# Kernel tuning notes

Hardware: AMD Instinct MI355X
Metric: run time of the kernel (lower is better)

The kernel has to match this reference:

```python
import jax, jax.numpy as jnp
import numpy as np

D_MODEL = 256
D_STATE = 64
D_CONV = 4
EXPAND = 2
HEADDIM = 64
D_INNER = EXPAND * D_MODEL            # 512
NHEADS = D_INNER // HEADDIM           # 8
D_XBC = D_INNER + 2 * D_STATE         # 640 (x, B, C; ngroups=1)
D_IN_PROJ = 2 * D_INNER + 2 * D_STATE + NHEADS  # 1160


def setup_inputs() -> dict:
    key = jax.random.key(0)
    ks = jax.random.split(key, 8)
    x = jax.random.normal(ks[0], (64, 5000, 12), jnp.float32)
    W_in = jax.random.normal(ks[1], (D_MODEL, D_IN_PROJ), jnp.float32) * 0.02
    conv_w = jax.random.normal(ks[2], (D_XBC, D_CONV), jnp.float32) * 0.1
    conv_b = jnp.zeros((D_XBC,), jnp.float32)
    A_log = jnp.log(jax.random.uniform(ks[3], (NHEADS,), jnp.float32, 1.0, 16.0))
    dt_bias = jax.random.normal(ks[4], (NHEADS,), jnp.float32) * 0.1
    D = jnp.ones((NHEADS,), jnp.float32)
    norm_w = jnp.ones((D_INNER,), jnp.float32)
    W_out = jax.random.normal(ks[5], (D_INNER, D_MODEL), jnp.float32) * 0.02
    return {"x": x, "W_in": W_in, "conv_w": conv_w, "conv_b": conv_b,
            "A_log": A_log, "dt_bias": dt_bias, "D": D,
            "norm_w": norm_w, "W_out": W_out}


def _mamba2(u, W_in, conv_w, conv_b, A_log, dt_bias, D, norm_w, W_out):
    b, l, _ = u.shape
    zxbcdt = u @ W_in                                   # (b,l,1160)
    z = zxbcdt[..., :D_INNER]                           # (b,l,512)
    xBC = zxbcdt[..., D_INNER:D_INNER + D_XBC]          # (b,l,640)
    dt = zxbcdt[..., D_INNER + D_XBC:]                  # (b,l,8)
    # causal depthwise conv1d (kernel 4) + SiLU
    xp = jnp.pad(xBC, ((0, 0), (D_CONV - 1, 0), (0, 0)))
    xBC = sum(xp[:, k:k + l, :] * conv_w[:, k] for k in range(D_CONV)) + conv_b
    xBC = jax.nn.silu(xBC)
    xs = xBC[..., :D_INNER].reshape(b, l, NHEADS, HEADDIM)
    Bm = xBC[..., D_INNER:D_INNER + D_STATE]            # (b,l,64)
    Cm = xBC[..., D_INNER + D_STATE:]                   # (b,l,64)
    dt = jax.nn.softplus(dt + dt_bias)                  # (b,l,h)
    A = -jnp.exp(A_log)                                 # (h,)

    def step(h, inp):
        x_t, dt_t, B_t, C_t = inp                       # (b,h,p),(b,h),(b,n),(b,n)
        decay = jnp.exp(dt_t * A)                       # (b,h)
        h = h * decay[..., None, None] + (dt_t[..., None] * x_t)[..., None] * B_t[:, None, None, :]
        y = jnp.einsum('bhpn,bn->bhp', h, C_t)
        return h, y

    h0 = jnp.zeros((b, NHEADS, HEADDIM, D_STATE), u.dtype)
    _, ys = jax.lax.scan(step, h0, (xs.transpose(1, 0, 2, 3), dt.transpose(1, 0, 2),
                                    Bm.transpose(1, 0, 2), Cm.transpose(1, 0, 2)))
    y = ys.transpose(1, 0, 2, 3) + D[None, None, :, None] * xs   # D skip, per head
    y = y.reshape(b, l, D_INNER)
    # RMSNormGated: gate then rmsnorm
    y = y * jax.nn.silu(z)
    y = y * jax.lax.rsqrt(jnp.mean(y * y, axis=-1, keepdims=True) + 1e-5) * norm_w
    return y @ W_out                                    # (b,l,256)


def reference(x, W_in, conv_w, conv_b, A_log, dt_bias, D, norm_w, W_out):
    b = x.shape[0]
    u = x.reshape(b, 250, 240)                          # 'b (t p1) f -> b t (p1 f)'
    u = jnp.pad(u, ((0, 0), (0, 0), (0, D_MODEL - 240)))
    y = _mamba2(u, W_in, conv_w, conv_b, A_log, dt_bias, D, norm_w, W_out)
    y = jax.nn.selu(y)                                  # AlphaDropout is identity at eval
    y = y[..., :240]
    return y.reshape(b, 5000, 12)
```

## Files before the change

### kernel.cpp

```cpp
#include <hip/hip_runtime.h>
#include <cstdint>
#include <cstddef>

#define D_MODEL 256
#define D_STATE 64
#define HEADDIM 64
#define D_INNER 512
#define NHEADS 8
#define D_XBC 640
#define NPROJ 1160
#define ZXW 1152
#define BATCH 64
#define SEQ 250
#define ROWS (BATCH * SEQ)
#define KIN 240
#define KPAD 256
#define NPAD 1216
#define TPAD 256

typedef __bf16 bf16x8 __attribute__((ext_vector_type(8)));
typedef float f32x4 __attribute__((ext_vector_type(4)));

__device__ __forceinline__ float readlane_f(float v, int lane) {
    return __uint_as_float(__builtin_amdgcn_readlane(__float_as_uint(v), lane));
}
__device__ __forceinline__ float silu_f(float x) { return x * (1.f / (1.f + __expf(-x))); }
__device__ __forceinline__ unsigned short bf16_rne(float f) {
    unsigned int u = __float_as_uint(f);
    u += 0x7fff + ((u >> 16) & 1);
    return (unsigned short)(u >> 16);
}
__device__ __forceinline__ float bf2f(unsigned short u) {
    return __uint_as_float(((unsigned int)u) << 16);
}
__device__ __forceinline__ unsigned int pack2(float a, float b) {
    return (unsigned int)bf16_rne(a) | ((unsigned int)bf16_rne(b) << 16);
}

__global__ __launch_bounds__(256) void cast_w_kernel(const float* __restrict__ Win,
                                                     unsigned short* __restrict__ bt_bf) {
    int idx = blockIdx.x * 256 + threadIdx.x;
    int n = idx >> 8, k = idx & 255;
    float v = (n < NPROJ && k < KIN) ? Win[k * NPROJ + n] : 0.f;
    bt_bf[idx] = bf16_rne(v);
}

#define SA 40
__global__ __launch_bounds__(256) void gemm1_mfma(const float* __restrict__ X,
                                                  const unsigned short* __restrict__ Bt,
                                                  unsigned short* __restrict__ Czx,
                                                  float* __restrict__ dtraw) {
    __shared__ unsigned short As[128 * SA];
    __shared__ unsigned short Bs[64 * SA];
    const int tid = threadIdx.x;
    const int lane = tid & 63, wave = tid >> 6;
    const int wm = wave >> 1, wn = wave & 1;
    const int q = lane >> 4, l15 = lane & 15;
    const int rowBase = blockIdx.y * 128, colBase = blockIdx.x * 64;
    f32x4 acc[4][2] = {};

    const int sr = tid >> 2;
    const int sc = (tid & 3) * 8;

    for (int k0 = 0; k0 < KPAD; k0 += 32) {
        const int kseg = k0 + sc;
        const bool kv = kseg < KIN;
        {
            unsigned short tmp[8] = {0, 0, 0, 0, 0, 0, 0, 0};
            if (kv) {
                const float* xr = X + (size_t)(rowBase + sr) * KIN + kseg;
                float4 a = *(const float4*)&xr[0];
                float4 b2 = *(const float4*)&xr[4];
                tmp[0] = bf16_rne(a.x); tmp[1] = bf16_rne(a.y);
                tmp[2] = bf16_rne(a.z); tmp[3] = bf16_rne(a.w);
                tmp[4] = bf16_rne(b2.x); tmp[5] = bf16_rne(b2.y);
                tmp[6] = bf16_rne(b2.z); tmp[7] = bf16_rne(b2.w);
            }
            *(uint4*)&As[sr * SA + sc] = *(uint4*)tmp;
        }
        {
            unsigned short tmp[8] = {0, 0, 0, 0, 0, 0, 0, 0};
            if (kv) {
                const float* xr = X + (size_t)(rowBase + sr + 64) * KIN + kseg;
                float4 a = *(const float4*)&xr[0];
                float4 b2 = *(const float4*)&xr[4];
                tmp[0] = bf16_rne(a.x); tmp[1] = bf16_rne(a.y);
                tmp[2] = bf16_rne(a.z); tmp[3] = bf16_rne(a.w);
                tmp[4] = bf16_rne(b2.x); tmp[5] = bf16_rne(b2.y);
                tmp[6] = bf16_rne(b2.z); tmp[7] = bf16_rne(b2.w);
            }
            *(uint4*)&As[(sr + 64) * SA + sc] = *(uint4*)tmp;
        }
        *(float4*)&Bs[sr * SA + sc] =
            *(const float4*)&Bt[(size_t)(colBase + sr) * KPAD + k0 + sc];
        __syncthreads();

        bf16x8 bfr[2];
#pragma unroll
        for (int nt = 0; nt < 2; nt++)
            bfr[nt] = *(const bf16x8*)&Bs[(wn * 32 + nt * 16 + l15) * SA + q * 8];
#pragma unroll
        for (int mt = 0; mt < 4; mt++) {
            bf16x8 afr = *(const bf16x8*)&As[(wm * 64 + mt * 16 + l15) * SA + q * 8];
#pragma unroll
            for (int nt = 0; nt < 2; nt++)
                acc[mt][nt] = __builtin_amdgcn_mfma_f32_16x16x32_bf16(afr, bfr[nt],
                                                                      acc[mt][nt], 0, 0, 0);
        }
        __syncthreads();
    }
#pragma unroll
    for (int mt = 0; mt < 4; mt++) {
        int grow0 = rowBase + wm * 64 + mt * 16 + q * 4;
#pragma unroll
        for (int nt = 0; nt < 2; nt++) {
            int gcol = colBase + wn * 32 + nt * 16 + l15;
            if (gcol < ZXW) {
#pragma unroll
                for (int reg = 0; reg < 4; reg++) {
                    unsigned int u = bf16_rne(acc[mt][nt][reg]);
                    unsigned int partner = (unsigned int)__shfl_xor((int)u, 1, 64);
                    if ((l15 & 1) == 0)
                        *(unsigned int*)&Czx[(size_t)(grow0 + reg) * ZXW + gcol] =
                            u | (partner << 16);
                }
            } else if (gcol < NPROJ) {
#pragma unroll
                for (int reg = 0; reg < 4; reg++)
                    dtraw[(size_t)(grow0 + reg) * NHEADS + (gcol - ZXW)] = acc[mt][nt][reg];
            }
        }
    }
}

#define CT_IN_STR 68
#define CT_TR_STR 70
__global__ __launch_bounds__(256) void conv_kernel(const unsigned short* __restrict__ zxbc,
                                                   const float* __restrict__ dtraw,
                                                   const float* __restrict__ conv_w,
                                                   const float* __restrict__ conv_b,
                                                   const float* __restrict__ dt_bias,
                                                   unsigned short* __restrict__ xc_bf,
                                                   unsigned short* __restrict__ xcT_bf,
                                                   float* __restrict__ dtp) {
    const int b = blockIdx.x;
    const int t0 = blockIdx.z * 64;
    if (blockIdx.y == 10) {
        for (int it = threadIdx.x; it < 512; it += 256) {
            int h = it & 7;
            int t = t0 + (it >> 3);
            if (t < SEQ) {
                float v = dtraw[(size_t)(b * SEQ + t) * NHEADS + h] + dt_bias[h];
                dtp[(size_t)(b * SEQ + t) * NHEADS + h] =
                    (v > 20.f) ? v : __logf(1.f + __expf(v));
            }
        }
        return;
    }
    __shared__ float In[67 * CT_IN_STR];
    __shared__ unsigned short OutT[64 * CT_TR_STR];
    const int cg = blockIdx.y;
    const int tid = threadIdx.x;
    const int lane = tid & 63;
    const int w = tid >> 6;
    const int ch = cg * 64 + lane;

    for (int r = w; r < 67; r += 4) {
        int t = t0 - 3 + r;
        float v = (t >= 0 && t < SEQ)
                      ? bf2f(zxbc[(size_t)(b * SEQ + t) * ZXW + D_INNER + ch])
                      : 0.f;
        In[r * CT_IN_STR + lane] = v;
    }
    __syncthreads();
    const float w0 = conv_w[ch * 4 + 0], w1 = conv_w[ch * 4 + 1];
    const float w2 = conv_w[ch * 4 + 2], w3 = conv_w[ch * 4 + 3];
    const float bias = conv_b[ch];
    unsigned short vals[16];
#pragma unroll
    for (int i = 0; i < 16; i++) {
        int tt = w * 16 + i;
        float acc = fmaf(w3, In[(tt + 3) * CT_IN_STR + lane],
                    fmaf(w2, In[(tt + 2) * CT_IN_STR + lane],
                    fmaf(w1, In[(tt + 1) * CT_IN_STR + lane],
                    fmaf(w0, In[tt * CT_IN_STR + lane], bias))));
        float sv = silu_f(acc);
        unsigned short bv = (t0 + tt < SEQ) ? bf16_rne(sv) : (unsigned short)0;
        vals[i] = bv;
        OutT[lane * CT_TR_STR + tt] = bv;
    }
#pragma unroll
    for (int i = 0; i < 16; i++) {
        int tt = w * 16 + i;
        if (t0 + tt < SEQ)
            xc_bf[(size_t)(b * SEQ + t0 + tt) * D_XBC + ch] = vals[i];
    }
    __syncthreads();
    unsigned short* dstbase = xcT_bf + ((size_t)b * D_XBC + cg * 64) * TPAD + t0;
#pragma unroll
    for (int i = 0; i < 16; i++) {
        int c2 = w * 16 + i;
        dstbase[(size_t)c2 * TPAD + lane] = OutT[c2 * CT_TR_STR + lane];
    }
}

#define LSTR 72
__global__ __launch_bounds__(256) void scan_intra(const unsigned short* __restrict__ xc_bf,
                                                  const unsigned short* __restrict__ xcT_bf,
                                                  const float* __restrict__ dtp,
                                                  const float* __restrict__ A_log,
                                                  const float* __restrict__ Dvec,
                                                  unsigned short* __restrict__ yout_bf,
                                                  unsigned short* __restrict__ st_g) {
    __shared__ unsigned short C_l[64 * LSTR];
    __shared__ unsigned short BP_l[64 * LSTR];
    __shared__ unsigned short XT_l[64 * LSTR];
    __shared__ float cs_s[64], dts_s[64], fws_s[64];

    const int blk = blockIdx.x;
    const int bh = blk >> 2, c = blk & 3;
    const int b = bh >> 3, h = bh & 7;
    const int tid = threadIdx.x;
    const int lane = tid & 63, w = tid >> 6;
    const int q = lane >> 4, l15 = lane & 15;
    const int t0 = c * 64;
    const float A = -__expf(A_log[h]);
    const float Dh = Dvec[h];

    const int r = tid >> 2, c0 = (tid & 3) * 16;

    {
        if (t0 + r < SEQ) {
            const unsigned short* rowp = xc_bf + (size_t)(b * SEQ + t0 + r) * D_XBC;
            *(uint4*)&C_l[r * LSTR + c0] = *(const uint4*)&rowp[D_INNER + D_STATE + c0];
            *(uint4*)&C_l[r * LSTR + c0 + 8] =
                *(const uint4*)&rowp[D_INNER + D_STATE + c0 + 8];
            *(uint4*)&BP_l[r * LSTR + c0] = *(const uint4*)&rowp[D_INNER + c0];
            *(uint4*)&BP_l[r * LSTR + c0 + 8] = *(const uint4*)&rowp[D_INNER + c0 + 8];
        } else {
            uint4 z = {0, 0, 0, 0};
            *(uint4*)&C_l[r * LSTR + c0] = z;
            *(uint4*)&C_l[r * LSTR + c0 + 8] = z;
            *(uint4*)&BP_l[r * LSTR + c0] = z;
            *(uint4*)&BP_l[r * LSTR + c0 + 8] = z;
        }
        const unsigned short* xrow =
            xcT_bf + ((size_t)b * D_XBC + h * HEADDIM + r) * TPAD + t0;
        *(uint4*)&XT_l[r * LSTR + c0] = *(const uint4*)&xrow[c0];
        *(uint4*)&XT_l[r * LSTR + c0 + 8] = *(const uint4*)&xrow[c0 + 8];
    }
    uint4 braw0, braw1;
    {
        const unsigned short* brow =
            xcT_bf + ((size_t)b * D_XBC + D_INNER + r) * TPAD + t0 + c0;
        braw0 = *(const uint4*)&brow[0];
        braw1 = *(const uint4*)&brow[8];
    }
    if (w == 0) {
        int t = lane;
        float dtv = (t0 + t < SEQ) ? dtp[(size_t)(b * SEQ + t0 + t) * NHEADS + h] : 0.f;
        float csv = dtv * A;
#pragma unroll
        for (int o = 1; o < 64; o <<= 1) {
            float u = __shfl_up(csv, o, 64);
            if (lane >= o) csv += u;
        }
        float tot = readlane_f(csv, 63);
        cs_s[t] = csv;
        dts_s[t] = dtv;
        fws_s[t] = dtv * __expf(tot - csv);
    }
    __syncthreads();

    f32x4 g[4] = {};
#pragma unroll
    for (int k0 = 0; k0 < 64; k0 += 32) {
        bf16x8 ca = *(const bf16x8*)&C_l[(w * 16 + l15) * LSTR + k0 + q * 8];
#pragma unroll
        for (int nt = 0; nt < 4; nt++) {
            bf16x8 bb = *(const bf16x8*)&BP_l[(nt * 16 + l15) * LSTR + k0 + q * 8];
            g[nt] = __builtin_amdgcn_mfma_f32_16x16x32_bf16(ca, bb, g[nt], 0, 0, 0);
        }
    }
    __syncthreads();

    {
        unsigned short tmp[16];
        const unsigned short* rp = (const unsigned short*)&braw0;
#pragma unroll
        for (int j = 0; j < 8; j++) tmp[j] = bf16_rne(bf2f(rp[j]) * fws_s[c0 + j]);
        rp = (const unsigned short*)&braw1;
#pragma unroll
        for (int j = 0; j < 8; j++) tmp[8 + j] = bf16_rne(bf2f(rp[j]) * fws_s[c0 + 8 + j]);
        *(uint4*)&C_l[r * LSTR + c0] = *(uint4*)&tmp[0];
        *(uint4*)&C_l[r * LSTR + c0 + 8] = *(uint4*)&tmp[8];
    }
#pragma unroll
    for (int nt = 0; nt < 4; nt++) {
#pragma unroll
        for (int rr = 0; rr < 4; rr++) {
            int t = w * 16 + q * 4 + rr;
            int s = nt * 16 + l15;
            float pv = 0.f;
            if (s <= t) {
                pv = g[nt][rr] * __expf(cs_s[t] - cs_s[s]) * dts_s[s];
                if (s == t) pv += Dh;
            }
            unsigned int u = bf16_rne(pv);
            unsigned int partner = (unsigned int)__shfl_xor((int)u, 1, 64);
            if ((l15 & 1) == 0)
                *(unsigned int*)&BP_l[t * LSTR + nt * 16 + l15] = u | (partner << 16);
        }
    }
    __syncthreads();

    f32x4 y[4] = {};
#pragma unroll
    for (int k0 = 0; k0 < 64; k0 += 32) {
        bf16x8 pa = *(const bf16x8*)&BP_l[(w * 16 + l15) * LSTR + k0 + q * 8];
#pragma unroll
        for (int nt = 0; nt < 4; nt++) {
            bf16x8 xb = *(const bf16x8*)&XT_l[(nt * 16 + l15) * LSTR + k0 + q * 8];
            y[nt] = __builtin_amdgcn_mfma_f32_16x16x32_bf16(pa, xb, y[nt], 0, 0, 0);
        }
    }
    if (c < 3) {
        f32x4 st[4] = {};
#pragma unroll
        for (int k0 = 0; k0 < 64; k0 += 32) {
            bf16x8 xa = *(const bf16x8*)&XT_l[(w * 16 + l15) * LSTR + k0 + q * 8];
#pragma unroll
            for (int nt = 0; nt < 4; nt++) {
                bf16x8 bwb = *(const bf16x8*)&C_l[(nt * 16 + l15) * LSTR + k0 + q * 8];
                st[nt] = __builtin_amdgcn_mfma_f32_16x16x32_bf16(xa, bwb, st[nt], 0, 0, 0);
            }
        }
        unsigned short* stc = st_g + ((size_t)(bh * 3 + c)) * 4096;
#pragma unroll
        for (int nt = 0; nt < 4; nt++)
#pragma unroll
            for (int rr = 0; rr < 4; rr++) {
                unsigned int u = bf16_rne(st[nt][rr]);
                unsigned int partner = (unsigned int)__shfl_xor((int)u, 1, 64);
                if ((l15 & 1) == 0)
                    *(unsigned int*)&stc[(w * 16 + q * 4 + rr) * 64 + nt * 16 + l15] =
                        u | (partner << 16);
            }
    }
#pragma unroll
    for (int nt = 0; nt < 4; nt++)
#pragma unroll
        for (int rr = 0; rr < 4; rr++) {
            int t = w * 16 + q * 4 + rr;
            if (t0 + t < SEQ) {
                int p = nt * 16 + l15;
                unsigned int u = bf16_rne(y[nt][rr]);
                unsigned int partner = (unsigned int)__shfl_xor((int)u, 1, 64);
                if ((l15 & 1) == 0)
                    *(unsigned int*)&yout_bf[(size_t)(b * SEQ + t0 + t) * D_INNER +
                                             h * HEADDIM + p] = u | (partner << 16);
            }
        }
}

__global__ __launch_bounds__(256) void scan_inter(const unsigned short* __restrict__ xc_bf,
                                                  const float* __restrict__ dtp,
                                                  const float* __restrict__ A_log,
                                                  unsigned short* __restrict__ yout_bf,
                                                  const unsigned short* __restrict__ st_g) {
    __shared__ unsigned short C_l[64 * LSTR];
    __shared__ unsigned short h_l[64 * LSTR];
    __shared__ float cs_s[64];
    __shared__ float csum[4];

    const int blk = blockIdx.x;
    const int bh = blk / 3, c = (blk - bh * 3) + 1;
    const int b = bh >> 3, h = bh & 7;
    const int tid = threadIdx.x;
    const int lane = tid & 63, w = tid >> 6;
    const int q = lane >> 4, l15 = lane & 15;
    const int t0 = c * 64;
    const float A = -__expf(A_log[h]);

    {
        int t = lane;
        int gt = w * 64 + t;
        float dtv = (gt < SEQ) ? dtp[(size_t)(b * SEQ + gt) * NHEADS + h] : 0.f;
        float csv = dtv * A;
#pragma unroll
        for (int o = 1; o < 64; o <<= 1) {
            float u = __shfl_up(csv, o, 64);
            if (lane >= o) csv += u;
        }
        if (w == c) cs_s[t] = csv;
        if (lane == 63) csum[w] = csv;
    }
    {
        int r = tid >> 2, c0 = (tid & 3) * 16;
        if (t0 + r < SEQ) {
            const unsigned short* rowp = xc_bf + (size_t)(b * SEQ + t0 + r) * D_XBC;
            *(uint4*)&C_l[r * LSTR + c0] = *(const uint4*)&rowp[D_INNER + D_STATE + c0];
            *(uint4*)&C_l[r * LSTR + c0 + 8] =
                *(const uint4*)&rowp[D_INNER + D_STATE + c0 + 8];
        } else {
            uint4 z = {0, 0, 0, 0};
            *(uint4*)&C_l[r * LSTR + c0] = z;
            *(uint4*)&C_l[r * LSTR + c0 + 8] = z;
        }
    }
    __syncthreads();

    {
        float wgt[3];
        for (int cp = 0; cp < c; cp++) {
            float s = 0.f;
            for (int j = cp + 1; j < c; j++) s += csum[j];
            wgt[cp] = __expf(s);
        }
        const unsigned short* stb = st_g + (size_t)bh * 3 * 4096;
        for (int i = tid; i < 4096; i += 256) {
            float acc = 0.f;
            for (int cp = 0; cp < c; cp++) acc += wgt[cp] * bf2f(stb[cp * 4096 + i]);
            h_l[(i >> 6) * LSTR + (i & 63)] = bf16_rne(acc);
        }
    }
    __syncthreads();

    f32x4 in[4] = {};
#pragma unroll
    for (int k0 = 0; k0 < 64; k0 += 32) {
        bf16x8 ca = *(const bf16x8*)&C_l[(w * 16 + l15) * LSTR + k0 + q * 8];
#pragma unroll
        for (int nt = 0; nt < 4; nt++) {
            bf16x8 hb = *(const bf16x8*)&h_l[(nt * 16 + l15) * LSTR + k0 + q * 8];
            in[nt] = __builtin_amdgcn_mfma_f32_16x16x32_bf16(ca, hb, in[nt], 0, 0, 0);
        }
    }
#pragma unroll
    for (int nt = 0; nt < 4; nt++)
#pragma unroll
        for (int r = 0; r < 4; r++) {
            int t = w * 16 + q * 4 + r;
            if (t0 + t < SEQ) {
                int p = nt * 16 + l15;
                size_t ai = (size_t)(b * SEQ + t0 + t) * D_INNER + h * HEADDIM + p;
                float alpha = __expf(cs_s[t]);
                float nv = bf2f(yout_bf[ai]) + alpha * in[nt][r];
                unsigned int u = bf16_rne(nv);
                unsigned int partner = (unsigned int)__shfl_xor((int)u, 1, 64);
                if ((l15 & 1) == 0)
                    *(unsigned int*)&yout_bf[ai] = u | (partner << 16);
            }
        }
}

__global__ __launch_bounds__(256) void wcast_kernel(const float* __restrict__ Wout,
                                                    unsigned short* __restrict__ wt_bf) {
    int idx = blockIdx.x * 256 + threadIdx.x;
    int n = idx & 255, k = idx >> 8;
    wt_bf[n * D_INNER + k] = bf16_rne(Wout[k * D_MODEL + n]);
}

__global__ __launch_bounds__(256) void gate_kernel(const unsigned short* __restrict__ yout_bf,
                                                   const unsigned short* __restrict__ zxbc,
                                                   const float* __restrict__ norm_w,
                                                   unsigned short* __restrict__ g_bf) {
    const int wid = threadIdx.x >> 6, lane = threadIdx.x & 63;
    const int row = blockIdx.x * 4 + wid;
    const unsigned short* yr = yout_bf + (size_t)row * D_INNER;
    const unsigned short* zr = zxbc + (size_t)row * ZXW;
    const int c0 = lane * 8;
    uint4 yp = *(const uint4*)&yr[c0];
    uint4 zp = *(const uint4*)&zr[c0];
    const unsigned short* ys = (const unsigned short*)&yp;
    const unsigned short* zs = (const unsigned short*)&zp;
    float g[8];
#pragma unroll
    for (int i = 0; i < 8; i++) g[i] = bf2f(ys[i]) * silu_f(bf2f(zs[i]));
    float s = 0.f;
#pragma unroll
    for (int i = 0; i < 8; i++) s = fmaf(g[i], g[i], s);
#pragma unroll
    for (int o = 32; o; o >>= 1) s += __shfl_xor(s, o, 64);
    float rms = rsqrtf(s * (1.f / 512.f) + 1e-5f);
    float4 w0 = *(const float4*)&norm_w[c0], w1 = *(const float4*)&norm_w[c0 + 4];
    uint4 pk;
    pk.x = pack2(g[0] * rms * w0.x, g[1] * rms * w0.y);
    pk.y = pack2(g[2] * rms * w0.z, g[3] * rms * w0.w);
    pk.z = pack2(g[4] * rms * w1.x, g[5] * rms * w1.y);
    pk.w = pack2(g[6] * rms * w1.z, g[7] * rms * w1.w);
    *(uint4*)&g_bf[(size_t)row * D_INNER + c0] = pk;
}

__global__ __launch_bounds__(256) void gemm2_mfma(const unsigned short* __restrict__ A,
                                                  const unsigned short* __restrict__ Bt,
                                                  float* __restrict__ out) {
    __shared__ unsigned short As[128 * SA];
    __shared__ unsigned short Bs[64 * SA];
    const int tid = threadIdx.x;
    const int lane = tid & 63, wave = tid >> 6;
    const int wm = wave >> 1, wn = wave & 1;
    const int q = lane >> 4, l15 = lane & 15;
    const int rowBase = blockIdx.y * 128, colBase = blockIdx.x * 64;
    f32x4 acc[4][2] = {};

    const int sr = tid >> 2;
    const int sc = (tid & 3) * 8;

    for (int k0 = 0; k0 < D_INNER; k0 += 32) {
        *(float4*)&As[sr * SA + sc] =
            *(const float4*)&A[(size_t)(rowBase + sr) * D_INNER + k0 + sc];
        *(float4*)&As[(sr + 64) * SA + sc] =
            *(const float4*)&A[(size_t)(rowBase + sr + 64) * D_INNER + k0 + sc];
        *(float4*)&Bs[sr * SA + sc] =
            *(const float4*)&Bt[(size_t)(colBase + sr) * D_INNER + k0 + sc];
        __syncthreads();

        bf16x8 bfr[2];
#pragma unroll
        for (int nt = 0; nt < 2; nt++)
            bfr[nt] = *(const bf16x8*)&Bs[(wn * 32 + nt * 16 + l15) * SA + q * 8];
#pragma unroll
        for (int mt = 0; mt < 4; mt++) {
            bf16x8 afr = *(const bf16x8*)&As[(wm * 64 + mt * 16 + l15) * SA + q * 8];
#pragma unroll
            for (int nt = 0; nt < 2; nt++)
                acc[mt][nt] = __builtin_amdgcn_mfma_f32_16x16x32_bf16(afr, bfr[nt],
                                                                      acc[mt][nt], 0, 0, 0);
        }
        __syncthreads();
    }
    const float SC = 1.0507009873554805f, AL = 1.6732632423543772f;
#pragma unroll
    for (int mt = 0; mt < 4; mt++) {
        int grow = rowBase + wm * 64 + mt * 16 + q * 4;
#pragma unroll
        for (int nt = 0; nt < 2; nt++) {
            int gcol = colBase + wn * 32 + nt * 16 + l15;
            if (gcol < 240) {
#pragma unroll
                for (int reg = 0; reg < 4; reg++) {
                    float v = acc[mt][nt][reg];
                    v = (v > 0.f) ? SC * v : SC * AL * (__expf(v) - 1.f);
                    out[(size_t)(grow + reg) * 240 + gcol] = v;
                }
            }
        }
    }
}

extern "C" void kernel_launch(void* const* d_in, const int* in_sizes, int n_in,
                              void* d_out, int out_size, void* d_ws, size_t ws_size,
                              hipStream_t stream) {
    const float* x = (const float*)d_in[0];
    const float* W_in = (const float*)d_in[1];
    const float* conv_w = (const float*)d_in[2];
    const float* conv_b = (const float*)d_in[3];
    const float* A_log = (const float*)d_in[4];
    const float* dt_bias = (const float*)d_in[5];
    const float* Dv = (const float*)d_in[6];
    const float* norm_w = (const float*)d_in[7];
    const float* W_out = (const float*)d_in[8];
    float* out = (float*)d_out;

    unsigned short* us = (unsigned short*)d_ws;
    unsigned short* zxbc_bf = us;
    unsigned short* xc_bf = zxbc_bf + (size_t)ROWS * ZXW;
    unsigned short* xcT_bf = xc_bf + (size_t)ROWS * D_XBC;
    unsigned short* yout_bf = xcT_bf + (size_t)BATCH * D_XBC * TPAD;
    unsigned short* st_g = yout_bf + (size_t)ROWS * D_INNER;
    unsigned short* bt_bf = st_g + (size_t)512 * 3 * 4096;
    unsigned short* wt_bf = bt_bf + (size_t)NPAD * KPAD;
    unsigned short* g_bf = wt_bf + (size_t)D_MODEL * D_INNER;
    float* dtraw = (float*)(g_bf + (size_t)ROWS * D_INNER);
    float* dtp = dtraw + (size_t)ROWS * NHEADS;

    cast_w_kernel<<<dim3(NPAD * KPAD / 256), 256, 0, stream>>>(W_in, bt_bf);

    gemm1_mfma<<<dim3(NPAD / 64, ROWS / 128), 256, 0, stream>>>(x, bt_bf, zxbc_bf, dtraw);

    conv_kernel<<<dim3(BATCH, 11, 4), 256, 0, stream>>>(zxbc_bf, dtraw, conv_w, conv_b,
                                                        dt_bias, xc_bf, xcT_bf, dtp);

    scan_intra<<<dim3(BATCH * NHEADS * 4), 256, 0, stream>>>(xc_bf, xcT_bf, dtp, A_log, Dv,
                                                             yout_bf, st_g);

    scan_inter<<<dim3(BATCH * NHEADS * 3), 256, 0, stream>>>(xc_bf, dtp, A_log,
                                                             yout_bf, st_g);

    wcast_kernel<<<dim3(D_INNER * D_MODEL / 256), 256, 0, stream>>>(W_out, wt_bf);

    gate_kernel<<<dim3(ROWS / 4), 256, 0, stream>>>(yout_bf, zxbc_bf, norm_w, g_bf);

    gemm2_mfma<<<dim3(D_MODEL / 64, ROWS / 128), 256, 0, stream>>>(g_bf, wt_bf, out);
}
```

Before: 221.6 us.

## Restructure in-projection GEMM to keep A row tile in registers across all columns

The first GEMM changes from a 2D grid of 128x64 tiles into one block per 64 rows. Each block converts its X rows to bf16 once, holds the full K=256 A fragments in registers, and then loops over all 19 column tiles, staging each B tile in XOR-swizzled shared memory. This avoids re-reading and re-converting X for every column block and reduces LDS bank conflicts. In exchange the grid shrinks to 250 blocks, each working serially over 19 column tiles with two barriers per tile, which lowers parallelism and latency hiding.

```diff
diff --git a/kernel.cpp b/kernel.cpp
--- a/kernel.cpp
+++ b/kernel.cpp
@@ -45,89 +45,89 @@
     bt_bf[idx] = bf16_rne(v);
 }
 
-#define SA 40
+#define SB 272
 __global__ __launch_bounds__(256) void gemm1_mfma(const float* __restrict__ X,
                                                   const unsigned short* __restrict__ Bt,
                                                   unsigned short* __restrict__ Czx,
                                                   float* __restrict__ dtraw) {
-    __shared__ unsigned short As[128 * SA];
-    __shared__ unsigned short Bs[64 * SA];
+    __shared__ unsigned short S[64 * SB];
     const int tid = threadIdx.x;
-    const int lane = tid & 63, wave = tid >> 6;
-    const int wm = wave >> 1, wn = wave & 1;
+    const int lane = tid & 63, w = tid >> 6;
     const int q = lane >> 4, l15 = lane & 15;
-    const int rowBase = blockIdx.y * 128, colBase = blockIdx.x * 64;
-    f32x4 acc[4][2] = {};
-
-    const int sr = tid >> 2;
-    const int sc = (tid & 3) * 8;
-
-    for (int k0 = 0; k0 < KPAD; k0 += 32) {
-        const int kseg = k0 + sc;
-        const bool kv = kseg < KIN;
+    const int rowBase = blockIdx.x * 64;
+
+    {
+        const int r = tid >> 2, seg = tid & 3;
+        const float* xr = X + (size_t)(rowBase + r) * KIN;
+#pragma unroll
+        for (int i = 0; i < 15; i++) {
+            int c4 = seg * 15 + i;
+            float4 v = *(const float4*)&xr[c4 * 4];
+            unsigned short t4[4];
+            t4[0] = bf16_rne(v.x); t4[1] = bf16_rne(v.y);
+            t4[2] = bf16_rne(v.z); t4[3] = bf16_rne(v.w);
+            *(uint2*)&S[r * SB + c4 * 4] = *(uint2*)t4;
+        }
+        if (seg < 2) {
+            uint4 z = {0, 0, 0, 0};
+            *(uint4*)&S[r * SB + 240 + seg * 8] = z;
+        }
+    }
+    __syncthreads();
+    bf16x8 afr[8];
+#pragma unroll
+    for (int kk = 0; kk < 8; kk++)
+        afr[kk] = *(const bf16x8*)&S[(w * 16 + l15) * SB + kk * 32 + q * 8];
+    __syncthreads();
+
+    for (int j = 0; j < 19; j++) {
         {
-            unsigned short tmp[8] = {0, 0, 0, 0, 0, 0, 0, 0};
-            if (kv) {
-                const float* xr = X + (size_t)(rowBase + sr) * KIN + kseg;
-                float4 a = *(const float4*)&xr[0];
-                float4 b2 = *(const float4*)&xr[4];
-                tmp[0] = bf16_rne(a.x); tmp[1] = bf16_rne(a.y);
-                tmp[2] = bf16_rne(a.z); tmp[3] = bf16_rne(a.w);
-                tmp[4] = bf16_rne(b2.x); tmp[5] = bf16_rne(b2.y);
-                tmp[6] = bf16_rne(b2.z); tmp[7] = bf16_rne(b2.w);
-            }
-            *(uint4*)&As[sr * SA + sc] = *(uint4*)tmp;
-        }
-        {
-            unsigned short tmp[8] = {0, 0, 0, 0, 0, 0, 0, 0};
-            if (kv) {
-                const float* xr = X + (size_t)(rowBase + sr + 64) * KIN + kseg;
-                float4 a = *(const float4*)&xr[0];
-                float4 b2 = *(const float4*)&xr[4];
-                tmp[0] = bf16_rne(a.x); tmp[1] = bf16_rne(a.y);
-                tmp[2] = bf16_rne(a.z); tmp[3] = bf16_rne(a.w);
-                tmp[4] = bf16_rne(b2.x); tmp[5] = bf16_rne(b2.y);
-                tmp[6] = bf16_rne(b2.z); tmp[7] = bf16_rne(b2.w);
-            }
-            *(uint4*)&As[(sr + 64) * SA + sc] = *(uint4*)tmp;
-        }
-        *(float4*)&Bs[sr * SA + sc] =
-            *(const float4*)&Bt[(size_t)(colBase + sr) * KPAD + k0 + sc];
+            const int r = tid >> 2, seg = tid & 3;
+            const unsigned short* br = Bt + (size_t)(j * 64 + r) * KPAD;
+#pragma unroll
+            for (int i = 0; i < 8; i++) {
+                int c = seg * 8 + i * 32;
+                int cs = (c ^ ((r & 3) << 3));
+                *(uint4*)&S[r * SB + cs] = *(const uint4*)&br[c];
+            }
+        }
         __syncthreads();
-
-        bf16x8 bfr[2];
-#pragma unroll
-        for (int nt = 0; nt < 2; nt++)
-            bfr[nt] = *(const bf16x8*)&Bs[(wn * 32 + nt * 16 + l15) * SA + q * 8];
-#pragma unroll
-        for (int mt = 0; mt < 4; mt++) {
-            bf16x8 afr = *(const bf16x8*)&As[(wm * 64 + mt * 16 + l15) * SA + q * 8];
-#pragma unroll
-            for (int nt = 0; nt < 2; nt++)
-                acc[mt][nt] = __builtin_amdgcn_mfma_f32_16x16x32_bf16(afr, bfr[nt],
-                                                                      acc[mt][nt], 0, 0, 0);
+        f32x4 acc[4] = {};
+#pragma unroll
+        for (int kk = 0; kk < 8; kk++) {
+#pragma unroll
+            for (int nt = 0; nt < 4; nt++) {
+                int row = nt * 16 + l15;
+                int c = kk * 32 + q * 8;
+                int cs = (c ^ ((row & 3) << 3));
+                bf16x8 bfr = *(const bf16x8*)&S[row * SB + cs];
+                acc[nt] = __builtin_amdgcn_mfma_f32_16x16x32_bf16(afr[kk], bfr,
+                                                                  acc[nt], 0, 0, 0);
+            }
         }
         __syncthreads();
-    }
-#pragma unroll
-    for (int mt = 0; mt < 4; mt++) {
-        int grow0 = rowBase + wm * 64 + mt * 16 + q * 4;
-#pragma unroll
-        for (int nt = 0; nt < 2; nt++) {
-            int gcol = colBase + wn * 32 + nt * 16 + l15;
-            if (gcol < ZXW) {
+
+        if (j < 18) {
+#pragma unroll
+            for (int nt = 0; nt < 4; nt++) {
+                int gcol = j * 64 + nt * 16 + l15;
 #pragma unroll
                 for (int reg = 0; reg < 4; reg++) {
-                    unsigned int u = bf16_rne(acc[mt][nt][reg]);
+                    int grow = rowBase + w * 16 + q * 4 + reg;
+                    unsigned int u = bf16_rne(acc[nt][reg]);
                     unsigned int partner = (unsigned int)__shfl_xor((int)u, 1, 64);
                     if ((l15 & 1) == 0)
-                        *(unsigned int*)&Czx[(size_t)(grow0 + reg) * ZXW + gcol] =
+                        *(unsigned int*)&Czx[(size_t)grow * ZXW + gcol] =
                             u | (partner << 16);
                 }
-            } else if (gcol < NPROJ) {
-#pragma unroll
-                for (int reg = 0; reg < 4; reg++)
-                    dtraw[(size_t)(grow0 + reg) * NHEADS + (gcol - ZXW)] = acc[mt][nt][reg];
+            }
+        } else {
+            if (l15 < 8) {
+#pragma unroll
+                for (int reg = 0; reg < 4; reg++) {
+                    int grow = rowBase + w * 16 + q * 4 + reg;
+                    dtraw[(size_t)grow * NHEADS + l15] = acc[0][reg];
+                }
             }
         }
     }
@@ -492,6 +492,7 @@
     *(uint4*)&g_bf[(size_t)row * D_INNER + c0] = pk;
 }
 
+#define SA 40
 __global__ __launch_bounds__(256) void gemm2_mfma(const unsigned short* __restrict__ A,
                                                   const unsigned short* __restrict__ Bt,
                                                   float* __restrict__ out) {
@@ -577,7 +578,7 @@
 
     cast_w_kernel<<<dim3(NPAD * KPAD / 256), 256, 0, stream>>>(W_in, bt_bf);
 
-    gemm1_mfma<<<dim3(NPAD / 64, ROWS / 128), 256, 0, stream>>>(x, bt_bf, zxbc_bf, dtraw);
+    gemm1_mfma<<<dim3(ROWS / 64), 256, 0, stream>>>(x, bt_bf, zxbc_bf, dtraw);
 
     conv_kernel<<<dim3(BATCH, 11, 4), 256, 0, stream>>>(zxbc_bf, dtraw, conv_w, conv_b,
                                                         dt_bias, xc_bf, xcT_bf, dtp);
```

New measurement: 223.2 us. No clear change (+0.7%).
